# Kernel optimization log

Measured on AMD Instinct MI355X. Metric: run time of the kernel, lower is better.

Reference implementation:

```python
import jax, jax.numpy as jnp
import numpy as np

MARGIN = 0.5
SCALE = 64.0
EPS = 1e-12  # matches torch F.normalize default eps


def setup_inputs() -> dict:
    key = jax.random.key(0)
    k1, k2, k3 = jax.random.split(key, 3)
    B, D, C = 1024, 512, 100000
    features = jax.random.normal(k1, (B, D), dtype=jnp.float32)
    labels = jax.random.randint(k2, (B,), 0, C, dtype=jnp.int64)
    # xavier_uniform for [C, D] weight: bound = sqrt(6/(C+D))
    bound = np.sqrt(6.0 / (C + D)).astype(np.float32)
    weight = jax.random.uniform(k3, (C, D), dtype=jnp.float32, minval=-bound, maxval=bound)
    return {"features": features, "labels": labels, "weight": weight}


def _l2norm(x):
    # F.normalize(dim=1): x / max(||x||, eps)
    n = jnp.sqrt(jnp.sum(x * x, axis=1, keepdims=True))
    return x / jnp.maximum(n, EPS)


def reference(features, labels, weight):
    f = _l2norm(features)              # [B, D]
    w = _l2norm(weight)                # [C, D]
    cos_theta = f @ w.T                # [B, C]
    B = features.shape[0]
    rows = jnp.arange(B)
    # subtract margin at the label position only (no one-hot materialization)
    cos_m = cos_theta.at[rows, labels].add(-MARGIN)
    logits = cos_m * SCALE
    logZ = jax.nn.logsumexp(logits, axis=1)        # [B]
    tgt = logits[rows, labels]                     # [B]
    loss = jnp.mean(logZ - tgt)
    return loss
```

## Files before the change

### kernel.cpp

```cpp
#include <hip/hip_runtime.h>
#include <hip/hip_bf16.h>
#include <hip/hip_fp8.h>
#include <stdint.h>

#define B_ROWS 1024
#define DIM    512
#define C_CLS  100000
#define C_PAD  100352
#define NT     784
#define NT_PER_XCD 98
#define MT     8
#define NPAD   (C_PAD - C_CLS)

using f32x4  = __attribute__((ext_vector_type(4))) float;

#define AS1(p) ((const __attribute__((address_space(1))) uint32_t*)(p))
#define AS3(p) ((__attribute__((address_space(3))) uint32_t*)(p))
#define SBAR()   __builtin_amdgcn_s_barrier()
#define VMCNT0() asm volatile("s_waitcnt vmcnt(0)" ::: "memory")

static __device__ __forceinline__ uint32_t f2fp8(float f) {
    __hip_fp8_e4m3 q(f);
    return (uint32_t)q.__x;
}
static __device__ __forceinline__ float fp82f(uint32_t b) {
    __hip_fp8_e4m3 h;
    h.__x = (__hip_fp8_storage_t)b;
    return (float)h;
}

__global__ __launch_bounds__(256) void normalize_rows(
    const float* __restrict__ src, uint8_t* __restrict__ dst, int nvalid, int ntotal)
{
    const int row  = blockIdx.x * 4 + (threadIdx.x >> 6);
    const int lane = threadIdx.x & 63;
    if (row >= ntotal) return;
    uint2* d2 = reinterpret_cast<uint2*>(dst + (size_t)row * DIM);
    if (row >= nvalid) { d2[lane] = make_uint2(0u, 0u); return; }
    const float4* s4 = reinterpret_cast<const float4*>(src + (size_t)row * DIM);
    const float4 a = s4[lane * 2], b = s4[lane * 2 + 1];
    float ss = a.x*a.x + a.y*a.y + a.z*a.z + a.w*a.w
             + b.x*b.x + b.y*b.y + b.z*b.z + b.w*b.w;
    #pragma unroll
    for (int k = 1; k < 64; k <<= 1) ss += __shfl_xor(ss, k);
    const float inv = 1.0f / fmaxf(sqrtf(ss), 1e-12f);
    uint2 o;
    o.x = f2fp8(a.x*inv) | (f2fp8(a.y*inv) << 8) | (f2fp8(a.z*inv) << 16) | (f2fp8(a.w*inv) << 24);
    o.y = f2fp8(b.x*inv) | (f2fp8(b.y*inv) << 8) | (f2fp8(b.z*inv) << 16) | (f2fp8(b.w*inv) << 24);
    d2[lane] = o;
}

__global__ __launch_bounds__(256, 3) void gemm_lse(
    const uint8_t* __restrict__ A,
    const uint8_t* __restrict__ W,
    float* __restrict__ ps)
{
    __shared__ __align__(16) uint8_t lds[2][128 * 64];

    const int tid  = threadIdx.x;
    const int lane = tid & 63;
    const int wid  = tid >> 6;
    const int wm   = wid >> 1;
    const int wn   = wid & 1;

    const int b     = blockIdx.x;
    const int xcd   = b & 7;
    const int j     = b >> 3;
    const int ntile = xcd * NT_PER_XCD + (j >> 3);
    const int mtile = j & 7;

    const uint8_t* Abase = A + (size_t)mtile * 128 * DIM;
    const uint8_t* Bbase = W + (size_t)ntile * 128 * DIM;

    const int rr = tid >> 2;
    const int cc = ((((tid & 3) << 1) ^ (rr & 6)) << 3);

    auto stage = [&](int kt) {
        const uint8_t* As = Abase + (size_t)rr * DIM + kt * 64 + cc;
        const uint8_t* Bs = Bbase + (size_t)rr * DIM + kt * 64 + cc;
        __builtin_amdgcn_global_load_lds(AS1(As),            AS3(&lds[0][tid * 16]),        16, 0, 0);
        __builtin_amdgcn_global_load_lds(AS1(As + 64 * DIM), AS3(&lds[0][4096 + tid * 16]), 16, 0, 0);
        __builtin_amdgcn_global_load_lds(AS1(Bs),            AS3(&lds[1][tid * 16]),        16, 0, 0);
        __builtin_amdgcn_global_load_lds(AS1(Bs + 64 * DIM), AS3(&lds[1][4096 + tid * 16]), 16, 0, 0);
    };

    const int l15 = lane & 15;
    const int uhi = lane >> 4;

    long aF[4][2], bF[4][2];
    f32x4 acc[4][4] = {};

    auto ldA = [&](int mi, int ks) {
        const int row = wm * 64 + mi * 16 + l15;
        const int v   = ((ks << 2) | uhi) ^ (row & 6);
        return *reinterpret_cast<const long*>(&lds[0][row * 64 + v * 8]);
    };
    auto ldB = [&](int ni, int ks) {
        const int row = wn * 64 + ni * 16 + l15;
        const int v   = ((ks << 2) | uhi) ^ (row & 6);
        return *reinterpret_cast<const long*>(&lds[1][row * 64 + v * 8]);
    };

    stage(0);

    #pragma unroll 1
    for (int kt = 0; kt < 8; ++kt) {
        VMCNT0(); SBAR();
        #pragma unroll
        for (int mi = 0; mi < 4; ++mi) { aF[mi][0] = ldA(mi, 0); aF[mi][1] = ldA(mi, 1); }
        #pragma unroll
        for (int ni = 0; ni < 4; ++ni) { bF[ni][0] = ldB(ni, 0); bF[ni][1] = ldB(ni, 1); }
        #pragma unroll
        for (int ks = 0; ks < 2; ++ks)
            #pragma unroll
            for (int mi = 0; mi < 4; ++mi)
                #pragma unroll
                for (int ni = 0; ni < 4; ++ni)
                    acc[mi][ni] = __builtin_amdgcn_mfma_f32_16x16x32_fp8_fp8(
                        aF[mi][ks], bF[ni][ks], acc[mi][ni], 0, 0, 0);
        SBAR();
        if (kt < 7) stage(kt + 1);
    }

    __syncthreads();
    float* red = reinterpret_cast<float*>(&lds[0][0]);
    #pragma unroll
    for (int mi = 0; mi < 4; ++mi) {
        #pragma unroll
        for (int r = 0; r < 4; ++r) {
            float s = __expf(fmaf(acc[mi][0][r], 64.0f, -64.0f))
                    + __expf(fmaf(acc[mi][1][r], 64.0f, -64.0f))
                    + __expf(fmaf(acc[mi][2][r], 64.0f, -64.0f))
                    + __expf(fmaf(acc[mi][3][r], 64.0f, -64.0f));
            #pragma unroll
            for (int k = 1; k < 16; k <<= 1) s += __shfl_xor(s, k);
            if (l15 == 0) red[(wm * 64 + mi * 16 + uhi * 4 + r) * 2 + wn] = s;
        }
    }
    __syncthreads();
    if (tid < 128)
        ps[(size_t)ntile * B_ROWS + mtile * 128 + tid] = red[tid * 2] + red[tid * 2 + 1];
}

__global__ __launch_bounds__(256) void finalize(
    const float* __restrict__ ps,
    const uint8_t* __restrict__ fb, const uint8_t* __restrict__ wb,
    const int* __restrict__ labels, float* __restrict__ row_loss)
{
    const int row = blockIdx.x;
    const int t   = threadIdx.x;
    const int lab = labels[row];

    const uint8_t* frow = fb + (size_t)row * DIM;
    const uint8_t* wrow = wb + (size_t)lab * DIM;
    uint32_t fa = *reinterpret_cast<const uint16_t*>(frow + 2 * t);
    uint32_t wa = *reinterpret_cast<const uint16_t*>(wrow + 2 * t);
    float d = fp82f(fa & 0xffu) * fp82f(wa & 0xffu)
            + fp82f(fa >> 8)    * fp82f(wa >> 8);
    #pragma unroll
    for (int k = 1; k < 64; k <<= 1) d += __shfl_xor(d, k);

    float s = 0.0f;
    for (int i = t; i < NT; i += 256) s += ps[(size_t)i * B_ROWS + row];
    #pragma unroll
    for (int k = 1; k < 64; k <<= 1) s += __shfl_xor(s, k);

    __shared__ float sd[4], ssm[4];
    if ((t & 63) == 0) { sd[t >> 6] = d; ssm[t >> 6] = s; }
    __syncthreads();
    if (t == 0) {
        const float dt = sd[0] + sd[1] + sd[2] + sd[3];
        float S = ssm[0] + ssm[1] + ssm[2] + ssm[3];
        const float lt = 64.0f * dt;
        S += expf(lt - 96.0f) - expf(lt - 64.0f) - (float)NPAD * expf(-64.0f);
        row_loss[row] = 64.0f + logf(S) - (lt - 32.0f);
    }
}

__global__ __launch_bounds__(256) void mean_k(const float* __restrict__ rl, float* __restrict__ out)
{
    const int t = threadIdx.x;
    float s = 0.0f;
    for (int i = t; i < B_ROWS; i += 256) s += rl[i];
    #pragma unroll
    for (int k = 1; k < 64; k <<= 1) s += __shfl_xor(s, k);
    __shared__ float r4[4];
    if ((t & 63) == 0) r4[t >> 6] = s;
    __syncthreads();
    if (t == 0) out[0] = (r4[0] + r4[1] + r4[2] + r4[3]) * (1.0f / B_ROWS);
}

extern "C" void kernel_launch(void* const* d_in, const int* in_sizes, int n_in,
                              void* d_out, int out_size, void* d_ws, size_t ws_size,
                              hipStream_t stream)
{
    const float* features = (const float*)d_in[0];
    const int*   labels   = (const int*)d_in[1];
    const float* weight   = (const float*)d_in[2];

    char* ws = (char*)d_ws;
    uint8_t* wb = (uint8_t*)ws;
    uint8_t* fb = (uint8_t*)(ws + (size_t)C_PAD * DIM);
    float*   psum = (float*)(ws + (size_t)C_PAD * DIM + (size_t)B_ROWS * DIM);
    float*   rl = psum + (size_t)NT * B_ROWS;

    normalize_rows<<<C_PAD / 4, 256, 0, stream>>>(weight, wb, C_CLS, C_PAD);
    normalize_rows<<<B_ROWS / 4, 256, 0, stream>>>(features, fb, B_ROWS, B_ROWS);
    gemm_lse<<<NT * MT, 256, 0, stream>>>(fb, wb, psum);
    finalize<<<B_ROWS, 256, 0, stream>>>(psum, fb, wb, labels, rl);
    mean_k<<<1, 256, 0, stream>>>(rl, (float*)d_out);
}
```

Baseline: 136.7 us.

## Use 16x16x128 scaled FP8 MFMA with K=128 tiles in GEMM

Measured after the change: 129.7 us (median of 2 runs). -5.1%, faster.

```diff
diff --git a/kernel.cpp b/kernel.cpp
--- a/kernel.cpp
+++ b/kernel.cpp
@@ -12,7 +12,9 @@
 #define MT     8
 #define NPAD   (C_PAD - C_CLS)
 
-using f32x4  = __attribute__((ext_vector_type(4))) float;
+using f32x4 = __attribute__((ext_vector_type(4))) float;
+using i32x4 = __attribute__((ext_vector_type(4))) int;
+using i32x8 = __attribute__((ext_vector_type(8))) int;
 
 #define AS1(p) ((const __attribute__((address_space(1))) uint32_t*)(p))
 #define AS3(p) ((__attribute__((address_space(3))) uint32_t*)(p))
@@ -55,7 +57,7 @@
     const uint8_t* __restrict__ W,
     float* __restrict__ ps)
 {
-    __shared__ __align__(16) uint8_t lds[2][128 * 64];
+    __shared__ __align__(16) uint8_t lds[2][128 * 128];
 
     const int tid  = threadIdx.x;
     const int lane = tid & 63;
@@ -72,54 +74,52 @@
     const uint8_t* Abase = A + (size_t)mtile * 128 * DIM;
     const uint8_t* Bbase = W + (size_t)ntile * 128 * DIM;
 
-    const int rr = tid >> 2;
-    const int cc = ((((tid & 3) << 1) ^ (rr & 6)) << 3);
-
     auto stage = [&](int kt) {
-        const uint8_t* As = Abase + (size_t)rr * DIM + kt * 64 + cc;
-        const uint8_t* Bs = Bbase + (size_t)rr * DIM + kt * 64 + cc;
-        __builtin_amdgcn_global_load_lds(AS1(As),            AS3(&lds[0][tid * 16]),        16, 0, 0);
-        __builtin_amdgcn_global_load_lds(AS1(As + 64 * DIM), AS3(&lds[0][4096 + tid * 16]), 16, 0, 0);
-        __builtin_amdgcn_global_load_lds(AS1(Bs),            AS3(&lds[1][tid * 16]),        16, 0, 0);
-        __builtin_amdgcn_global_load_lds(AS1(Bs + 64 * DIM), AS3(&lds[1][4096 + tid * 16]), 16, 0, 0);
+        #pragma unroll
+        for (int p = 0; p < 4; ++p) {
+            const int u   = tid + p * 256;
+            const int row = u >> 3;
+            const int sub = (u & 7) ^ (row & 7);
+            const uint8_t* As = Abase + (size_t)row * DIM + kt * 128 + sub * 16;
+            const uint8_t* Bs = Bbase + (size_t)row * DIM + kt * 128 + sub * 16;
+            __builtin_amdgcn_global_load_lds(AS1(As), AS3(&lds[0][u * 16]), 16, 0, 0);
+            __builtin_amdgcn_global_load_lds(AS1(Bs), AS3(&lds[1][u * 16]), 16, 0, 0);
+        }
     };
 
     const int l15 = lane & 15;
     const int uhi = lane >> 4;
 
-    long aF[4][2], bF[4][2];
+    i32x8 aF[4], bF[4];
     f32x4 acc[4][4] = {};
 
-    auto ldA = [&](int mi, int ks) {
-        const int row = wm * 64 + mi * 16 + l15;
-        const int v   = ((ks << 2) | uhi) ^ (row & 6);
-        return *reinterpret_cast<const long*>(&lds[0][row * 64 + v * 8]);
+    auto ldfrag = [&](const uint8_t* base, int row) -> i32x8 {
+        const int swz = row & 7;
+        const i32x4 lo = *reinterpret_cast<const i32x4*>(base + row * 128 + (((uhi << 1) | 0) ^ swz) * 16);
+        const i32x4 hi = *reinterpret_cast<const i32x4*>(base + row * 128 + (((uhi << 1) | 1) ^ swz) * 16);
+        i32x8 r;
+        r[0] = lo[0]; r[1] = lo[1]; r[2] = lo[2]; r[3] = lo[3];
+        r[4] = hi[0]; r[5] = hi[1]; r[6] = hi[2]; r[7] = hi[3];
+        return r;
     };
-    auto ldB = [&](int ni, int ks) {
-        const int row = wn * 64 + ni * 16 + l15;
-        const int v   = ((ks << 2) | uhi) ^ (row & 6);
-        return *reinterpret_cast<const long*>(&lds[1][row * 64 + v * 8]);
-    };
 
     stage(0);
 
     #pragma unroll 1
-    for (int kt = 0; kt < 8; ++kt) {
+    for (int kt = 0; kt < 4; ++kt) {
         VMCNT0(); SBAR();
         #pragma unroll
-        for (int mi = 0; mi < 4; ++mi) { aF[mi][0] = ldA(mi, 0); aF[mi][1] = ldA(mi, 1); }
-        #pragma unroll
-        for (int ni = 0; ni < 4; ++ni) { bF[ni][0] = ldB(ni, 0); bF[ni][1] = ldB(ni, 1); }
-        #pragma unroll
-        for (int ks = 0; ks < 2; ++ks)
+        for (int mi = 0; mi < 4; ++mi) aF[mi] = ldfrag(&lds[0][0], wm * 64 + mi * 16 + l15);
+        #pragma unroll
+        for (int ni = 0; ni < 4; ++ni) bF[ni] = ldfrag(&lds[1][0], wn * 64 + ni * 16 + l15);
+        #pragma unroll
+        for (int mi = 0; mi < 4; ++mi)
             #pragma unroll
-            for (int mi = 0; mi < 4; ++mi)
-                #pragma unroll
-                for (int ni = 0; ni < 4; ++ni)
-                    acc[mi][ni] = __builtin_amdgcn_mfma_f32_16x16x32_fp8_fp8(
-                        aF[mi][ks], bF[ni][ks], acc[mi][ni], 0, 0, 0);
+            for (int ni = 0; ni < 4; ++ni)
+                acc[mi][ni] = __builtin_amdgcn_mfma_scale_f32_16x16x128_f8f6f4(
+                    aF[mi], bF[ni], acc[mi][ni], 0, 0, 0, 127, 0, 127);
         SBAR();
-        if (kt < 7) stage(kt + 1);
+        if (kt < 3) stage(kt + 1);
     }
 
     __syncthreads();
```
